# Kernel tuning notes

Measured on AMD Instinct MI355X. Metric: run time of the kernel, lower is better.

The kernel has to match this reference:

```python
import jax, jax.numpy as jnp
import numpy as np

N_HEADS = 8
N_GROUPS = 32
EPS = 1e-6


def setup_inputs() -> dict:
    key = jax.random.key(0)
    ks = jax.random.split(key, 8)
    b, c, n, K = 2, 512, 1024, 64
    x = jax.random.normal(ks[0], (b, c, n), dtype=jnp.float32)
    valid_mask = jax.random.randint(ks[1], (n, K), 0, 2, dtype=jnp.int32)
    # ensure every query attends to at least one key (avoids all--inf softmax rows)
    valid_mask = valid_mask.at[:, 0].set(1)
    attend_idx = jax.random.randint(ks[2], (n, K), 0, n, dtype=jnp.int64)
    scale = 0.03
    return {
        "x": x,
        "valid_mask": valid_mask,
        "attend_idx": attend_idx,
        "gn_gamma": jnp.ones((c,), jnp.float32),
        "gn_beta": jnp.zeros((c,), jnp.float32),
        "wq": jax.random.normal(ks[3], (c, c), jnp.float32) * scale,
        "bq": jnp.zeros((c,), jnp.float32),
        "wk": jax.random.normal(ks[4], (c, c), jnp.float32) * scale,
        "bk": jnp.zeros((c,), jnp.float32),
        "wv": jax.random.normal(ks[5], (c, c), jnp.float32) * scale,
        "bv": jnp.zeros((c,), jnp.float32),
        "wo": jax.random.normal(ks[6], (c, c), jnp.float32) * scale,
        "bo": jnp.zeros((c,), jnp.float32),
    }


def _group_norm(x, gamma, beta):
    b, c, n = x.shape
    xr = x.reshape(b, N_GROUPS, c // N_GROUPS, n)
    mu = xr.mean(axis=(2, 3), keepdims=True)
    var = xr.var(axis=(2, 3), keepdims=True)
    h = ((xr - mu) * jax.lax.rsqrt(var + EPS)).reshape(b, c, n)
    return h * gamma[None, :, None] + beta[None, :, None]


def reference(x, valid_mask, attend_idx, gn_gamma, gn_beta,
              wq, bq, wk, bk, wv, bv, wo, bo):
    b, c, n = x.shape
    H = N_HEADS
    dh = c // H
    h = _group_norm(x, gn_gamma, gn_beta)
    # 1x1 Conv1d == per-node linear projection
    proj = lambda w, bias: jnp.einsum('oc,bcn->bon', w, h) + bias[None, :, None]
    q = proj(wq, bq).reshape(b, H, dh, n)
    k = proj(wk, bk).reshape(b, H, dh, n)
    v = proj(wv, bv).reshape(b, H, dh, n)
    # gather attendable keys/values per query: [b, H, nq, K, dh]
    kT = jnp.transpose(k, (0, 1, 3, 2))  # [b, H, n, dh]
    vT = jnp.transpose(v, (0, 1, 3, 2))
    keys = jnp.take(kT, attend_idx, axis=2)
    vals = jnp.take(vT, attend_idx, axis=2)
    # NOTE: sparse_forward uses beta=1 (no 1/sqrt(dh) scaling)
    w = jnp.einsum('bhqkc,bhcq->bhqk', keys, q)
    w = jnp.where(valid_mask[None, None] == 0, -jnp.inf, w)
    w = jax.nn.softmax(w, axis=-1)
    o = jnp.einsum('bhqk,bhqkc->bhqc', w, vals)  # [b, H, n, dh]
    # permute(0,3,1,2).reshape(b,c,n): channel layout is (dh, H)
    o = jnp.transpose(o, (0, 3, 1, 2)).reshape(b, c, n)
    out = x + jnp.einsum('oc,bcn->bon', wo, o) + bo[None, :, None]
    return out
```

## Files before the change

### kernel.cpp

```cpp
#include <hip/hip_runtime.h>
#include <hip/hip_bf16.h>

#define B_   2
#define C_   512
#define N_   1024
#define KK_  64
#define H_   8
#define DH_  64
#define NG_  32
#define MQKV 1536

typedef __attribute__((ext_vector_type(8))) short short8;
typedef __attribute__((ext_vector_type(4))) float f32x4;

__device__ __forceinline__ float ldf(const void* p, size_t i, int isbf) {
  return isbf ? __bfloat162float(((const __hip_bfloat16*)p)[i])
              : ((const float*)p)[i];
}
__device__ __forceinline__ unsigned short f2bfu(float f) {
  __hip_bfloat16 h = __float2bfloat16(f);
  unsigned short u; __builtin_memcpy(&u, &h, 2); return u;
}
__device__ __forceinline__ float bfu2f(unsigned short u) {
  return __uint_as_float(((unsigned)u) << 16);
}
__device__ __forceinline__ int detect_bf(const void* gamma) {
  return ((const unsigned*)gamma)[0] == 0x3F803F80u;
}
__device__ __forceinline__ uint4 ld8_bf(const void* w, size_t off, int isbf) {
  if (isbf) return *(const uint4*)((const unsigned short*)w + off);
  float4 a = *(const float4*)((const float*)w + off);
  float4 b = *(const float4*)((const float*)w + off + 4);
  uint4 u;
  u.x = (unsigned)f2bfu(a.x) | ((unsigned)f2bfu(a.y) << 16);
  u.y = (unsigned)f2bfu(a.z) | ((unsigned)f2bfu(a.w) << 16);
  u.z = (unsigned)f2bfu(b.x) | ((unsigned)f2bfu(b.y) << 16);
  u.w = (unsigned)f2bfu(b.z) | ((unsigned)f2bfu(b.w) << 16);
  return u;
}
__device__ __forceinline__ void dma16(const void* g, void* l) {
  __builtin_amdgcn_global_load_lds(
      (const __attribute__((address_space(1))) unsigned*)g,
      (__attribute__((address_space(3))) unsigned*)l, 16, 0, 0);
}
__device__ __forceinline__ float dot8(uint4 kv, const float* qf) {
  float s;
  s  = __uint_as_float(kv.x << 16) * qf[0] + __uint_as_float(kv.x & 0xffff0000u) * qf[1];
  s += __uint_as_float(kv.y << 16) * qf[2] + __uint_as_float(kv.y & 0xffff0000u) * qf[3];
  s += __uint_as_float(kv.z << 16) * qf[4] + __uint_as_float(kv.z & 0xffff0000u) * qf[5];
  s += __uint_as_float(kv.w << 16) * qf[6] + __uint_as_float(kv.w & 0xffff0000u) * qf[7];
  return s;
}

__global__ __launch_bounds__(256) void conv_k(
    const void* x, const void* wq, const void* wk, const void* wv, const void* wo,
    const void* gamma, unsigned short* __restrict__ wqkvS,
    unsigned short* __restrict__ woS, float2* __restrict__ part) {
  const int isbf = detect_bf(gamma);
  const int tid = threadIdx.x;
  const int t8 = blockIdx.x * 256 + tid;
  if (t8 < (MQKV * C_) / 8) {
    int e0 = t8 * 8;
    int m = e0 >> 9, c0 = e0 & 511;
    const void* src = (m < 512) ? wq : (m < 1024 ? wk : wv);
    *(uint4*)&wqkvS[e0] = ld8_bf(src, (size_t)(m & 511) * C_ + c0, isbf);
  } else if (woS != nullptr && t8 < (MQKV * C_) / 8 + (C_ * C_) / 8) {
    int e0 = (t8 - (MQKV * C_) / 8) * 8;
    *(uint4*)&woS[e0] = ld8_bf(wo, e0, isbf);
  }

  __shared__ float ssum[256], ssq[256];
  if (blockIdx.x < 256) {
    const size_t base = (size_t)blockIdx.x * 4096;
    float sum = 0.f, sq = 0.f;
    if (isbf) {
      const uint4* p = (const uint4*)((const unsigned short*)x + base);
      for (int t = tid; t < 512; t += 256) {
        uint4 u = p[t];
        unsigned wv4[4] = {u.x, u.y, u.z, u.w};
#pragma unroll
        for (int q = 0; q < 4; q++) {
          float a = __uint_as_float(wv4[q] << 16);
          float b = __uint_as_float(wv4[q] & 0xffff0000u);
          sum += a + b; sq += a * a + b * b;
        }
      }
    } else {
      const float4* p = (const float4*)((const float*)x + base);
      for (int t = tid; t < 1024; t += 256) {
        float4 v = p[t];
        sum += v.x + v.y + v.z + v.w;
        sq  += v.x * v.x + v.y * v.y + v.z * v.z + v.w * v.w;
      }
    }
    ssum[tid] = sum; ssq[tid] = sq;
    __syncthreads();
    for (int s = 128; s > 0; s >>= 1) {
      if (tid < s) { ssum[tid] += ssum[tid + s]; ssq[tid] += ssq[tid + s]; }
      __syncthreads();
    }
    if (tid == 0) part[blockIdx.x] = make_float2(ssum[0], ssq[0]);
  }
}

__global__ __launch_bounds__(256) void gn_apply_k(
    const void* x, const void* gamma, const void* beta,
    const float2* __restrict__ part, unsigned short* __restrict__ hT) {
  const int isbf = detect_bf(gamma);
  const int n0 = blockIdx.x * 64, c0 = blockIdx.y * 64, b = blockIdx.z;
  const int tid = threadIdx.x;
  __shared__ unsigned short Lt[64][72];
#pragma unroll
  for (int p = 0; p < 2; p++) {
    int idx = tid + p * 256;
    int cl = idx >> 3, seg = idx & 7;
    int c = c0 + cl;
    int bgi = (b * NG_ + (c >> 4)) * 4;
    float2 p0 = part[bgi], p1 = part[bgi + 1], p2 = part[bgi + 2], p3 = part[bgi + 3];
    float S = p0.x + p1.x + p2.x + p3.x;
    float Q = p0.y + p1.y + p2.y + p3.y;
    float mu = S * (1.f / 16384.f);
    float rs = rsqrtf(fmaxf(Q * (1.f / 16384.f) - mu * mu, 0.f) + 1e-6f);
    float ga = ldf(gamma, c, isbf), be = ldf(beta, c, isbf);
    size_t srow = ((size_t)b * C_ + c) * N_ + n0 + seg * 8;
    float v[8];
    if (isbf) {
      uint4 u = *(const uint4*)((const unsigned short*)x + srow);
      v[0] = __uint_as_float(u.x << 16); v[1] = __uint_as_float(u.x & 0xffff0000u);
      v[2] = __uint_as_float(u.y << 16); v[3] = __uint_as_float(u.y & 0xffff0000u);
      v[4] = __uint_as_float(u.z << 16); v[5] = __uint_as_float(u.z & 0xffff0000u);
      v[6] = __uint_as_float(u.w << 16); v[7] = __uint_as_float(u.w & 0xffff0000u);
    } else {
      float4 a = *(const float4*)((const float*)x + srow);
      float4 bb = *(const float4*)((const float*)x + srow + 4);
      v[0] = a.x; v[1] = a.y; v[2] = a.z; v[3] = a.w;
      v[4] = bb.x; v[5] = bb.y; v[6] = bb.z; v[7] = bb.w;
    }
#pragma unroll
    for (int e = 0; e < 8; e++)
      Lt[seg * 8 + e][cl] = f2bfu((v[e] - mu) * rs * ga + be);
  }
  __syncthreads();
#pragma unroll
  for (int p = 0; p < 2; p++) {
    int idx = tid + p * 256;
    int nl = idx >> 3, seg = idx & 7;
    uint4 v = *(const uint4*)&Lt[nl][seg * 8];
    *(uint4*)&hT[((size_t)b * N_ + n0 + nl) * C_ + c0 + seg * 8] = v;
  }
}

__global__ __launch_bounds__(256) void qkv_gemm_k(
    const unsigned short* __restrict__ wqkvS, const unsigned short* __restrict__ hT,
    const void* bq, const void* bk, const void* bv, const void* gamma,
    unsigned short* __restrict__ qkv) {
  const int isbf = detect_bf(gamma);
  __shared__ short As[8192], Bs[8192];
  const int tid = threadIdx.x;
  const int lane = tid & 63, wave = tid >> 6;
  const int wm = wave >> 1, wn = wave & 1;
  const int n0 = blockIdx.x * 64;
  const int m0 = blockIdx.y * 64;
  const int b  = blockIdx.z;
  const unsigned short* Bbase = hT + (size_t)b * N_ * C_;
  const void* bsrc = (m0 < 512) ? bq : (m0 < 1024 ? bk : bv);

  const int r = lane & 15, kh = (lane >> 4) << 3;
  const size_t arow = (size_t)(m0 + wave * 16 + r) * C_;
  const size_t brow = (size_t)(n0 + wave * 16 + r) * C_;
  short* Ad = &As[wave * 512];
  short* Bd = &Bs[wave * 512];

  f32x4 acc[2][2];
#pragma unroll
  for (int i = 0; i < 2; i++)
#pragma unroll
    for (int j = 0; j < 2; j++) acc[i][j] = (f32x4){0.f, 0.f, 0.f, 0.f};

#define STAGE_Q(bufv, k0v)                                              \
  { dma16(&wqkvS[arow + (k0v) + kh],      Ad + (bufv) * 4096);          \
    dma16(&wqkvS[arow + (k0v) + 32 + kh], Ad + (bufv) * 4096 + 2048);   \
    dma16(&Bbase[brow + (k0v) + kh],      Bd + (bufv) * 4096);          \
    dma16(&Bbase[brow + (k0v) + 32 + kh], Bd + (bufv) * 4096 + 2048); }

  STAGE_Q(0, 0);
  __syncthreads();
  int buf = 0;
  for (int t = 0; t < 8; ++t) {
    if (t < 7) STAGE_Q(buf ^ 1, (t + 1) * 64);
#pragma unroll
    for (int s = 0; s < 2; ++s) {
      const short8* Av = (const short8*)&As[buf * 4096 + s * 2048];
      const short8* Bv = (const short8*)&Bs[buf * 4096 + s * 2048];
      short8 af[2], bg[2];
#pragma unroll
      for (int i = 0; i < 2; i++) af[i] = Av[(wm * 2 + i) * 64 + lane];
#pragma unroll
      for (int j = 0; j < 2; j++) bg[j] = Bv[(wn * 2 + j) * 64 + lane];
#pragma unroll
      for (int i = 0; i < 2; i++)
#pragma unroll
        for (int j = 0; j < 2; j++)
          acc[i][j] = __builtin_amdgcn_mfma_f32_16x16x32_bf16(af[i], bg[j], acc[i][j], 0, 0, 0);
    }
    __syncthreads();
    buf ^= 1;
  }
#undef STAGE_Q

  const int mb = m0 + wm * 32;
#pragma unroll
  for (int i = 0; i < 2; i++) {
    int mrow0 = mb + i * 16 + ((lane >> 4) << 2);
    int mat = mrow0 >> 9, head = (mrow0 >> 6) & 7, d0 = mrow0 & 63;
    int br = mrow0 & 511;
    float b0 = ldf(bsrc, br, isbf),     b1 = ldf(bsrc, br + 1, isbf);
    float b2 = ldf(bsrc, br + 2, isbf), b3 = ldf(bsrc, br + 3, isbf);
#pragma unroll
    for (int j = 0; j < 2; j++) {
      int n = n0 + wn * 32 + j * 16 + (lane & 15);
      uint2 st;
      st.x = (unsigned)f2bfu(acc[i][j][0] + b0) | ((unsigned)f2bfu(acc[i][j][1] + b1) << 16);
      st.y = (unsigned)f2bfu(acc[i][j][2] + b2) | ((unsigned)f2bfu(acc[i][j][3] + b3) << 16);
      size_t dst = (size_t)mat * ((size_t)B_ * H_ * N_ * DH_) +
                   (((size_t)b * H_ + head) * N_ + n) * DH_ + d0;
      *(uint2*)&qkv[dst] = st;
    }
  }
}

__global__ __launch_bounds__(512) void attn_k(
    const unsigned short* __restrict__ qkv, const void* aidx,
    const int* __restrict__ vmask, unsigned short* __restrict__ ocT) {
  const int tid = threadIdx.x, w = tid >> 6, lane = tid & 63;
  const int b = blockIdx.x >> 10, qi = blockIdx.x & 1023;
  const int kg = lane >> 3, dq = lane & 7;

  const unsigned* aw = (const unsigned*)aidx;
  unsigned long long bal = __ballot(aw[2 * lane + 1] != 0u);
  const int is64 = (bal == 0ull);

  __shared__ float wl[8][64];
  __shared__ int   il[8][64];
  __shared__ int   vl[8][64];
  __shared__ unsigned short olds[512];

  const size_t S = (size_t)B_ * H_ * N_ * DH_;
  const unsigned short* qT = qkv;
  const unsigned short* kT = qkv + S;
  const unsigned short* vT = qkv + 2 * S;
  const size_t bh = ((size_t)b * H_ + w) * N_;

  uint4 qv = *(const uint4*)&qT[(bh + qi) * DH_ + dq * 8];
  float qf[8];
  qf[0] = __uint_as_float(qv.x << 16); qf[1] = __uint_as_float(qv.x & 0xffff0000u);
  qf[2] = __uint_as_float(qv.y << 16); qf[3] = __uint_as_float(qv.y & 0xffff0000u);
  qf[4] = __uint_as_float(qv.z << 16); qf[5] = __uint_as_float(qv.z & 0xffff0000u);
  qf[6] = __uint_as_float(qv.w << 16); qf[7] = __uint_as_float(qv.w & 0xffff0000u);

  const size_t ai = (size_t)qi * KK_ + lane;
  int idx = is64 ? (int)((const long long*)aidx)[ai] : ((const int*)aidx)[ai];
  idx &= (N_ - 1);
  il[w][lane] = idx;
  vl[w][lane] = vmask[ai];
  __threadfence_block();

  float own = 0.f;
#pragma unroll
  for (int p = 0; p < 8; p++) {
    int key = p * 8 + kg;
    int ix = il[w][key];
    uint4 kv = *(const uint4*)&kT[(bh + ix) * DH_ + dq * 8];
    float s = dot8(kv, qf);
    s += __shfl_xor(s, 1); s += __shfl_xor(s, 2); s += __shfl_xor(s, 4);
    if (dq == p) own = s;
  }
  const int keyown = dq * 8 + kg;
  const int valid = vl[w][keyown];
  float sc = valid ? own : -INFINITY;

  float m = sc;
#pragma unroll
  for (int off = 32; off > 0; off >>= 1) m = fmaxf(m, __shfl_xor(m, off));
  float e = valid ? __expf(sc - m) : 0.f;
  float sum = e;
#pragma unroll
  for (int off = 32; off > 0; off >>= 1) sum += __shfl_xor(sum, off);

  wl[w][keyown] = (sum > 0.f) ? (e / sum) : 0.f;
  __threadfence_block();

  const unsigned short* vbase = vT + bh * DH_;
  const int half = lane >> 5, dhp = lane & 31;
  float a0 = 0.f, a1 = 0.f;
#pragma unroll 8
  for (int ki = 0; ki < KK_ / 2; ki++) {
    int key = 2 * ki + half;
    float wgt = wl[w][key];
    unsigned uv = *(const unsigned*)&vbase[(size_t)il[w][key] * DH_ + 2 * dhp];
    a0 += wgt * __uint_as_float(uv << 16);
    a1 += wgt * __uint_as_float(uv & 0xffff0000u);
  }
  a0 += __shfl_xor(a0, 32);
  a1 += __shfl_xor(a1, 32);
  if (half == 0) {
    olds[(2 * dhp) * H_ + w]     = f2bfu(a0);
    olds[(2 * dhp + 1) * H_ + w] = f2bfu(a1);
  }
  __syncthreads();
  if (tid < 64) {
    uint4 vv = *(const uint4*)&olds[tid * 8];
    *(uint4*)&ocT[((size_t)b * N_ + qi) * C_ + tid * 8] = vv;
  }
}

__global__ __launch_bounds__(256) void out_gemm_k(
    const void* wo, const unsigned short* __restrict__ woS,
    const unsigned short* __restrict__ ocT,
    const void* bo, const void* __restrict__ x,
    const void* gamma, void* __restrict__ out) {
  const int isbf = detect_bf(gamma);
  __shared__ short As[8192], Bs[8192];
  const int tid = threadIdx.x;
  const int lane = tid & 63, wave = tid >> 6;
  const int wm = wave >> 1, wn = wave & 1;
  const int n0 = blockIdx.x * 64;
  const int m0 = blockIdx.y * 64;
  const int b  = blockIdx.z;
  const unsigned short* Bbase = ocT + (size_t)b * N_ * C_;
  const unsigned short* asrc = woS ? woS : (isbf ? (const unsigned short*)wo : nullptr);

  const int r = lane & 15, kh = (lane >> 4) << 3;
  const size_t arow = (size_t)(m0 + wave * 16 + r) * C_;
  const size_t brow = (size_t)(n0 + wave * 16 + r) * C_;
  short* Ad = &As[wave * 512];
  short* Bd = &Bs[wave * 512];

  f32x4 acc[2][2];
#pragma unroll
  for (int i = 0; i < 2; i++)
#pragma unroll
    for (int j = 0; j < 2; j++) acc[i][j] = (f32x4){0.f, 0.f, 0.f, 0.f};

#define STAGE_O(bufv, k0v)                                                        \
  { if (asrc) {                                                                   \
      dma16(&asrc[arow + (k0v) + kh],      Ad + (bufv) * 4096);                   \
      dma16(&asrc[arow + (k0v) + 32 + kh], Ad + (bufv) * 4096 + 2048);            \
    } else {                                                                      \
      *(uint4*)&As[(bufv) * 4096 + tid * 8]        = ld8_bf(wo, arow + (k0v) + kh, 0);      \
      *(uint4*)&As[(bufv) * 4096 + 2048 + tid * 8] = ld8_bf(wo, arow + (k0v) + 32 + kh, 0); \
    }                                                                             \
    dma16(&Bbase[brow + (k0v) + kh],      Bd + (bufv) * 4096);                    \
    dma16(&Bbase[brow + (k0v) + 32 + kh], Bd + (bufv) * 4096 + 2048); }

  STAGE_O(0, 0);
  __syncthreads();
  int buf = 0;
  for (int t = 0; t < 8; ++t) {
    if (t < 7) STAGE_O(buf ^ 1, (t + 1) * 64);
#pragma unroll
    for (int s = 0; s < 2; ++s) {
      const short8* Av = (const short8*)&As[buf * 4096 + s * 2048];
      const short8* Bv = (const short8*)&Bs[buf * 4096 + s * 2048];
      short8 af[2], bg[2];
#pragma unroll
      for (int i = 0; i < 2; i++) af[i] = Av[(wm * 2 + i) * 64 + lane];
#pragma unroll
      for (int j = 0; j < 2; j++) bg[j] = Bv[(wn * 2 + j) * 64 + lane];
#pragma unroll
      for (int i = 0; i < 2; i++)
#pragma unroll
        for (int j = 0; j < 2; j++)
          acc[i][j] = __builtin_amdgcn_mfma_f32_16x16x32_bf16(bg[j], af[i], acc[i][j], 0, 0, 0);
    }
    __syncthreads();
    buf ^= 1;
  }
#undef STAGE_O

#pragma unroll
  for (int i = 0; i < 2; i++) {
    int m = m0 + wm * 32 + i * 16 + (lane & 15);
    float bias = ldf(bo, m, isbf);
#pragma unroll
    for (int j = 0; j < 2; j++) {
      int nb = n0 + wn * 32 + j * 16 + ((lane >> 4) << 2);
      size_t oi = ((size_t)b * C_ + m) * N_ + nb;
      if (isbf) {
        const unsigned short* xp = (const unsigned short*)x;
        uint2 xv = *(const uint2*)&xp[oi];
        uint2 st;
        st.x = (unsigned)f2bfu(bfu2f((unsigned short)(xv.x & 0xffff)) + acc[i][j][0] + bias) |
               ((unsigned)f2bfu(bfu2f((unsigned short)(xv.x >> 16)) + acc[i][j][1] + bias) << 16);
        st.y = (unsigned)f2bfu(bfu2f((unsigned short)(xv.y & 0xffff)) + acc[i][j][2] + bias) |
               ((unsigned)f2bfu(bfu2f((unsigned short)(xv.y >> 16)) + acc[i][j][3] + bias) << 16);
        *(uint2*)&((unsigned short*)out)[oi] = st;
      } else {
        const float* xp = (const float*)x;
        float4 xv = *(const float4*)&xp[oi];
        float4 st;
        st.x = xv.x + acc[i][j][0] + bias;
        st.y = xv.y + acc[i][j][1] + bias;
        st.z = xv.z + acc[i][j][2] + bias;
        st.w = xv.w + acc[i][j][3] + bias;
        *(float4*)&((float*)out)[oi] = st;
      }
    }
  }
}

extern "C" void kernel_launch(void* const* d_in, const int* in_sizes, int n_in,
                              void* d_out, int out_size, void* d_ws, size_t ws_size,
                              hipStream_t stream) {
  const void* x     = d_in[0];
  const int*  vmask = (const int*)d_in[1];
  const void* aidx  = d_in[2];
  const void* gamma = d_in[3];
  const void* beta  = d_in[4];
  const void* wq = d_in[5],  *bq = d_in[6];
  const void* wk = d_in[7],  *bk = d_in[8];
  const void* wv = d_in[9],  *bv = d_in[10];
  const void* wo = d_in[11], *bo = d_in[12];

  unsigned short* qkv = (unsigned short*)d_ws;
  unsigned short* hT  = qkv + (size_t)3 * B_ * H_ * N_ * DH_;
  unsigned short* ocT = hT;
  unsigned short* wqkvS = (unsigned short*)d_out;
  float2* part = (float2*)((char*)d_out + (size_t)MQKV * C_ * 2);
  unsigned short* woS = nullptr;
  if (ws_size >= ((size_t)8 << 20) + (size_t)C_ * C_ * 2)
    woS = (unsigned short*)((char*)d_ws + ((size_t)8 << 20));

  conv_k<<<512, 256, 0, stream>>>(x, wq, wk, wv, wo, gamma, wqkvS, woS, part);
  gn_apply_k<<<dim3(N_ / 64, C_ / 64, B_), 256, 0, stream>>>(x, gamma, beta, part, hT);
  qkv_gemm_k<<<dim3(N_ / 64, MQKV / 64, B_), 256, 0, stream>>>(
      wqkvS, hT, bq, bk, bv, gamma, qkv);
  attn_k<<<B_ * N_, 512, 0, stream>>>(qkv, aidx, vmask, ocT);
  out_gemm_k<<<dim3(N_ / 64, C_ / 64, B_), 256, 0, stream>>>(
      wo, woS, ocT, bo, x, gamma, d_out);
}
```

Measured before the change: 130.8 us.

## Stage GEMM epilogues through LDS for coalesced stores; widen attention V gather

The QKV projection and output projection epilogues now write their accumulator tiles into shared memory first, then each thread stores 16 contiguous elements, so global writes are coalesced 128-bit stores instead of scattered 8- or 16-byte ones. The attention kernel reads the valid mask directly instead of through a shared array. It also splits the V gather across four key lanes with 8-byte loads per lane instead of two lanes with 4-byte loads. The cost is an extra barrier and LDS round-trip per GEMM block, plus more shuffles in the attention reduction.

```diff
diff --git a/kernel.cpp b/kernel.cpp
--- a/kernel.cpp
+++ b/kernel.cpp
@@ -208,24 +208,32 @@
   }
 #undef STAGE_Q
 
-  const int mb = m0 + wm * 32;
+  const int mat = m0 >> 9, head = (m0 >> 6) & 7;
+  const int brbase = m0 & 511;
+  unsigned short* Ls = (unsigned short*)As;
 #pragma unroll
   for (int i = 0; i < 2; i++) {
-    int mrow0 = mb + i * 16 + ((lane >> 4) << 2);
-    int mat = mrow0 >> 9, head = (mrow0 >> 6) & 7, d0 = mrow0 & 63;
-    int br = mrow0 & 511;
-    float b0 = ldf(bsrc, br, isbf),     b1 = ldf(bsrc, br + 1, isbf);
-    float b2 = ldf(bsrc, br + 2, isbf), b3 = ldf(bsrc, br + 3, isbf);
+    int d0 = wm * 32 + i * 16 + ((lane >> 4) << 2);
+    float b0 = ldf(bsrc, brbase + d0, isbf),     b1 = ldf(bsrc, brbase + d0 + 1, isbf);
+    float b2 = ldf(bsrc, brbase + d0 + 2, isbf), b3 = ldf(bsrc, brbase + d0 + 3, isbf);
 #pragma unroll
     for (int j = 0; j < 2; j++) {
-      int n = n0 + wn * 32 + j * 16 + (lane & 15);
+      int nloc = wn * 32 + j * 16 + (lane & 15);
       uint2 st;
       st.x = (unsigned)f2bfu(acc[i][j][0] + b0) | ((unsigned)f2bfu(acc[i][j][1] + b1) << 16);
       st.y = (unsigned)f2bfu(acc[i][j][2] + b2) | ((unsigned)f2bfu(acc[i][j][3] + b3) << 16);
-      size_t dst = (size_t)mat * ((size_t)B_ * H_ * N_ * DH_) +
-                   (((size_t)b * H_ + head) * N_ + n) * DH_ + d0;
-      *(uint2*)&qkv[dst] = st;
-    }
+      *(uint2*)&Ls[nloc * 68 + d0] = st;
+    }
+  }
+  __syncthreads();
+  {
+    const size_t S = (size_t)B_ * H_ * N_ * DH_;
+    int row = tid >> 2, chunk = (tid & 3) * 16;
+    uint4 v0 = *(const uint4*)&Ls[row * 68 + chunk];
+    uint4 v1 = *(const uint4*)&Ls[row * 68 + chunk + 8];
+    size_t dst = (size_t)mat * S + (((size_t)b * H_ + head) * N_ + n0 + row) * DH_ + chunk;
+    *(uint4*)&qkv[dst] = v0;
+    *(uint4*)&qkv[dst + 8] = v1;
   }
 }
 
@@ -242,7 +250,6 @@
 
   __shared__ float wl[8][64];
   __shared__ int   il[8][64];
-  __shared__ int   vl[8][64];
   __shared__ unsigned short olds[512];
 
   const size_t S = (size_t)B_ * H_ * N_ * DH_;
@@ -262,7 +269,6 @@
   int idx = is64 ? (int)((const long long*)aidx)[ai] : ((const int*)aidx)[ai];
   idx &= (N_ - 1);
   il[w][lane] = idx;
-  vl[w][lane] = vmask[ai];
   __threadfence_block();
 
   float own = 0.f;
@@ -276,7 +282,7 @@
     if (dq == p) own = s;
   }
   const int keyown = dq * 8 + kg;
-  const int valid = vl[w][keyown];
+  const int valid = vmask[(size_t)qi * KK_ + keyown];
   float sc = valid ? own : -INFINITY;
 
   float m = sc;
@@ -291,21 +297,27 @@
   __threadfence_block();
 
   const unsigned short* vbase = vT + bh * DH_;
-  const int half = lane >> 5, dhp = lane & 31;
-  float a0 = 0.f, a1 = 0.f;
+  const int q2 = lane >> 4, dhq = lane & 15;
+  float f0 = 0.f, f1 = 0.f, f2 = 0.f, f3 = 0.f;
 #pragma unroll 8
-  for (int ki = 0; ki < KK_ / 2; ki++) {
-    int key = 2 * ki + half;
+  for (int ki = 0; ki < KK_ / 4; ki++) {
+    int key = 4 * ki + q2;
     float wgt = wl[w][key];
-    unsigned uv = *(const unsigned*)&vbase[(size_t)il[w][key] * DH_ + 2 * dhp];
-    a0 += wgt * __uint_as_float(uv << 16);
-    a1 += wgt * __uint_as_float(uv & 0xffff0000u);
-  }
-  a0 += __shfl_xor(a0, 32);
-  a1 += __shfl_xor(a1, 32);
-  if (half == 0) {
-    olds[(2 * dhp) * H_ + w]     = f2bfu(a0);
-    olds[(2 * dhp + 1) * H_ + w] = f2bfu(a1);
+    uint2 uv = *(const uint2*)&vbase[(size_t)il[w][key] * DH_ + dhq * 4];
+    f0 += wgt * __uint_as_float(uv.x << 16);
+    f1 += wgt * __uint_as_float(uv.x & 0xffff0000u);
+    f2 += wgt * __uint_as_float(uv.y << 16);
+    f3 += wgt * __uint_as_float(uv.y & 0xffff0000u);
+  }
+  f0 += __shfl_xor(f0, 16); f0 += __shfl_xor(f0, 32);
+  f1 += __shfl_xor(f1, 16); f1 += __shfl_xor(f1, 32);
+  f2 += __shfl_xor(f2, 16); f2 += __shfl_xor(f2, 32);
+  f3 += __shfl_xor(f3, 16); f3 += __shfl_xor(f3, 32);
+  if (q2 == 0) {
+    olds[(dhq * 4 + 0) * H_ + w] = f2bfu(f0);
+    olds[(dhq * 4 + 1) * H_ + w] = f2bfu(f1);
+    olds[(dhq * 4 + 2) * H_ + w] = f2bfu(f2);
+    olds[(dhq * 4 + 3) * H_ + w] = f2bfu(f3);
   }
   __syncthreads();
   if (tid < 64) {
@@ -320,7 +332,9 @@
     const void* bo, const void* __restrict__ x,
     const void* gamma, void* __restrict__ out) {
   const int isbf = detect_bf(gamma);
-  __shared__ short As[8192], Bs[8192];
+  __shared__ short SMEM[16384];
+  short* As = SMEM;
+  short* Bs = SMEM + 8192;
   const int tid = threadIdx.x;
   const int lane = tid & 63, wave = tid >> 6;
   const int wm = wave >> 1, wn = wave & 1;
@@ -378,32 +392,52 @@
   }
 #undef STAGE_O
 
+  float* Ls = (float*)SMEM;
 #pragma unroll
   for (int i = 0; i < 2; i++) {
-    int m = m0 + wm * 32 + i * 16 + (lane & 15);
-    float bias = ldf(bo, m, isbf);
+    int cloc = wm * 32 + i * 16 + (lane & 15);
+    float bias = ldf(bo, m0 + cloc, isbf);
 #pragma unroll
     for (int j = 0; j < 2; j++) {
-      int nb = n0 + wn * 32 + j * 16 + ((lane >> 4) << 2);
-      size_t oi = ((size_t)b * C_ + m) * N_ + nb;
-      if (isbf) {
-        const unsigned short* xp = (const unsigned short*)x;
-        uint2 xv = *(const uint2*)&xp[oi];
-        uint2 st;
-        st.x = (unsigned)f2bfu(bfu2f((unsigned short)(xv.x & 0xffff)) + acc[i][j][0] + bias) |
-               ((unsigned)f2bfu(bfu2f((unsigned short)(xv.x >> 16)) + acc[i][j][1] + bias) << 16);
-        st.y = (unsigned)f2bfu(bfu2f((unsigned short)(xv.y & 0xffff)) + acc[i][j][2] + bias) |
-               ((unsigned)f2bfu(bfu2f((unsigned short)(xv.y >> 16)) + acc[i][j][3] + bias) << 16);
-        *(uint2*)&((unsigned short*)out)[oi] = st;
-      } else {
-        const float* xp = (const float*)x;
-        float4 xv = *(const float4*)&xp[oi];
+      int nbl = wn * 32 + j * 16 + ((lane >> 4) << 2);
+      float4 st;
+      st.x = acc[i][j][0] + bias; st.y = acc[i][j][1] + bias;
+      st.z = acc[i][j][2] + bias; st.w = acc[i][j][3] + bias;
+      *(float4*)&Ls[cloc * 68 + nbl] = st;
+    }
+  }
+  __syncthreads();
+  {
+    int row = tid >> 2, chunk = (tid & 3) * 16;
+    size_t oi = ((size_t)b * C_ + m0 + row) * N_ + n0 + chunk;
+    float v[16];
+#pragma unroll
+    for (int e = 0; e < 16; e++) v[e] = Ls[row * 68 + chunk + e];
+    if (isbf) {
+      const unsigned short* xp = (const unsigned short*)x;
+      uint4 x0 = *(const uint4*)&xp[oi];
+      uint4 x1 = *(const uint4*)&xp[oi + 8];
+      unsigned xs[8] = {x0.x, x0.y, x0.z, x0.w, x1.x, x1.y, x1.z, x1.w};
+      unsigned os[8];
+#pragma unroll
+      for (int q = 0; q < 8; q++) {
+        float lo = __uint_as_float(xs[q] << 16)         + v[2 * q];
+        float hi = __uint_as_float(xs[q] & 0xffff0000u) + v[2 * q + 1];
+        os[q] = (unsigned)f2bfu(lo) | ((unsigned)f2bfu(hi) << 16);
+      }
+      uint4 o0 = {os[0], os[1], os[2], os[3]}, o1 = {os[4], os[5], os[6], os[7]};
+      *(uint4*)&((unsigned short*)out)[oi] = o0;
+      *(uint4*)&((unsigned short*)out)[oi + 8] = o1;
+    } else {
+      const float* xp = (const float*)x;
+      float* op = (float*)out;
+#pragma unroll
+      for (int q = 0; q < 4; q++) {
+        float4 xv = *(const float4*)&xp[oi + q * 4];
         float4 st;
-        st.x = xv.x + acc[i][j][0] + bias;
-        st.y = xv.y + acc[i][j][1] + bias;
-        st.z = xv.z + acc[i][j][2] + bias;
-        st.w = xv.w + acc[i][j][3] + bias;
-        *(float4*)&((float*)out)[oi] = st;
+        st.x = xv.x + v[4 * q];     st.y = xv.y + v[4 * q + 1];
+        st.z = xv.z + v[4 * q + 2]; st.w = xv.w + v[4 * q + 3];
+        *(float4*)&op[oi + q * 4] = st;
       }
     }
   }
```

Measured after the change: 129.7 us (median of 2 runs). No clear change (-0.8%).
